# Kernel optimization log

Measured on AMD Instinct MI355X. Metric: run time of the kernel, lower is better.

## Reference

```python
import jax, jax.numpy as jnp
import numpy as np

HEADS = 8
EPS = 1e-5


def setup_inputs() -> dict:
    key = jax.random.key(0)
    ks = jax.random.split(key, 9)
    B, C, H, W = 4, 256, 128, 128
    s1 = 0.02
    inp = {
        "fmap": jax.random.normal(ks[0], (B, C, H, W), dtype=jnp.float32),
        "g": jnp.ones((C, 1, 1), dtype=jnp.float32),
        "wq1": jax.random.normal(ks[1], (C, C, 1, 1), dtype=jnp.float32) * s1,
        "wq2": jax.random.normal(ks[2], (C, 1, 3, 3), dtype=jnp.float32) * s1,
        "wk1": jax.random.normal(ks[3], (C, C, 1, 1), dtype=jnp.float32) * s1,
        "wk2": jax.random.normal(ks[4], (C, 1, 3, 3), dtype=jnp.float32) * s1,
        "wv1": jax.random.normal(ks[5], (C, C, 1, 1), dtype=jnp.float32) * s1,
        "wv2": jax.random.normal(ks[6], (C, 1, 3, 3), dtype=jnp.float32) * s1,
        "w_out": jax.random.normal(ks[7], (C, C, 1, 1), dtype=jnp.float32) * s1,
    }
    return inp


def _linear_attention(fmap, g, wq1, wq2, wk1, wk2, wv1, wv2, w_out):
    b, C, H, W = fmap.shape
    h = HEADS
    c = C // h          # head dim
    n = H * W           # tokens
    scale = c ** -0.5

    # channel LayerNorm over dim=-3 (C), learned gamma, no bias
    mean = jnp.mean(fmap, axis=1, keepdims=True)
    var = jnp.var(fmap, axis=1, keepdims=True)
    x = (fmap - mean) * jax.lax.rsqrt(var + EPS) * g[None]

    def proj(w1, w2):
        # 1x1 conv (no bias) then 3x3 depthwise conv (groups=C), SAME pad
        y = jnp.einsum('bchw,oc->bohw', x, w1[:, :, 0, 0])
        return jax.lax.conv_general_dilated(
            y, w2, window_strides=(1, 1), padding='SAME',
            dimension_numbers=('NCHW', 'OIHW', 'NCHW'),
            feature_group_count=C)

    q, k, v = proj(wq1, wq2), proj(wk1, wk2), proj(wv1, wv2)

    def to_heads(t):  # [b,C,H,W] -> [b*h, n, c]
        return t.reshape(b, h, c, n).transpose(0, 1, 3, 2).reshape(b * h, n, c)

    q, k, v = to_heads(q), to_heads(k), to_heads(v)

    q = jax.nn.softmax(q, axis=-1) * scale   # softmax over head dim
    k = jax.nn.softmax(k, axis=-2)            # softmax over tokens

    ctx = jnp.einsum('bnd,bne->bde', k, v)    # [b*h, c, c]
    out = jnp.einsum('bnd,bde->bne', q, ctx)  # [b*h, n, c]

    out = out.reshape(b, h, n, c).transpose(0, 1, 3, 2).reshape(b, C, H, W)
    out = jax.nn.silu(out)
    return jnp.einsum('bchw,oc->bohw', out, w_out[:, :, 0, 0])


def reference(fmap, g, wq1, wq2, wk1, wk2, wv1, wv2, w_out):
    return _linear_attention(fmap, g, wq1, wq2, wk1, wk2, wv1, wv2, w_out)
```

## Files before the change

kernel.cpp:

```cpp
#include <hip/hip_runtime.h>
#include <cmath>


#define B 4
#define C 256
#define Hh 128
#define Wd 128
#define HW (Hh*Wd)
#define HEADS 8
#define HD 32
#define OSCALE 256.0f
#define NSP 16

typedef _Float16 half_t;
typedef _Float16 f16x8 __attribute__((ext_vector_type(8)));
typedef float f32x4 __attribute__((ext_vector_type(4)));

__device__ __forceinline__ void gload_lds16(const half_t* g, half_t* l) {
  __builtin_amdgcn_global_load_lds((const __attribute__((address_space(1))) void*)g,
                                   (__attribute__((address_space(3))) void*)l, 16, 0, 0);
}

__global__ __launch_bounds__(256) void wcvt_all(const float* __restrict__ wq1,
                                                const float* __restrict__ wk1,
                                                const float* __restrict__ wv1,
                                                const float* __restrict__ wout,
                                                half_t* __restrict__ Wh,
                                                half_t* __restrict__ Woh,
                                                float* __restrict__ Sk) {
  int i = blockIdx.x * 256 + threadIdx.x;
  if (i < 65536) Wh[i] = (half_t)wq1[i];
  else if (i < 131072) Wh[i] = (half_t)wk1[i - 65536];
  else if (i < 196608) Wh[i] = (half_t)wv1[i - 131072];
  else Woh[i - 196608] = (half_t)wout[i - 196608];
  if (i < B * C) Sk[i] = 0.f;
}

__global__ __launch_bounds__(256) void ln2(const float* __restrict__ fmap,
                                           const float* __restrict__ g,
                                           half_t* __restrict__ Xh) {
  int b = blockIdx.y;
  int lane = threadIdx.x & 63;
  int gq = threadIdx.x >> 6;
  int px = blockIdx.x * 64 + lane;
  __shared__ float gs[C];
  __shared__ float sm1[4][64], sm2[4][64];
  gs[threadIdx.x] = g[threadIdx.x];
  const float* fp = fmap + ((size_t)b * C + gq * 64) * HW + px;
  float vbuf[64];
  float s = 0.f, s2 = 0.f;
#pragma unroll
  for (int j = 0; j < 64; ++j) {
    float v = fp[(size_t)j * HW];
    vbuf[j] = v;
    s += v; s2 = fmaf(v, v, s2);
  }
  sm1[gq][lane] = s; sm2[gq][lane] = s2;
  __syncthreads();
  float st = 0.f, st2 = 0.f;
#pragma unroll
  for (int q = 0; q < 4; ++q) { st += sm1[q][lane]; st2 += sm2[q][lane]; }
  float mean = st * (1.f / C);
  float var = st2 * (1.f / C) - mean * mean;
  float rstd = rsqrtf(var + 1e-5f);
  half_t* xp = Xh + ((size_t)b * HW + px) * 256 + gq * 64;
#pragma unroll
  for (int j0 = 0; j0 < 64; j0 += 8) {
    f16x8 v8;
#pragma unroll
    for (int jj = 0; jj < 8; ++jj)
      v8[jj] = (half_t)((vbuf[j0 + jj] - mean) * rstd * gs[gq * 64 + j0 + jj]);
    *(f16x8*)(xp + j0) = v8;
  }
}

__global__ __launch_bounds__(512) void gemm16w(const half_t* __restrict__ Xh,
                                               const half_t* __restrict__ Wh,
                                               half_t* __restrict__ Yh) {
  __shared__ __align__(16) char smem[65536];
  half_t* Xs0 = (half_t*)smem;
  half_t* Xs1 = (half_t*)(smem + 16384);
  half_t* Ws0 = (half_t*)(smem + 32768);
  half_t* Ws1 = (half_t*)(smem + 49152);
  const int tid = threadIdx.x;
  const int wave = tid >> 6, lane = tid & 63;
  const int lr = lane & 15, lq = lane >> 4;
  const int b = blockIdx.z;
  const int pix0 = blockIdx.x * 128;
  const int m0 = blockIdx.y * 128;
  const int wm = wave >> 1, wn = wave & 1;

  const half_t* xb = Xh + ((size_t)b * HW + pix0) * 256;
  const half_t* wb = Wh + (size_t)m0 * 256;

  f32x4 acc[2][4];
#pragma unroll
  for (int i = 0; i < 2; ++i)
#pragma unroll
    for (int j = 0; j < 4; ++j) { f32x4 z = {0.f, 0.f, 0.f, 0.f}; acc[i][j] = z; }

#pragma unroll
  for (int it = 0; it < 2; ++it) {
    int e = it * 512 + tid, r = e >> 3, c = e & 7;
    int go = (c ^ (r & 7)) << 3;
    gload_lds16(xb + (size_t)r * 256 + go, Xs0 + e * 8);
    gload_lds16(wb + (size_t)r * 256 + go, Ws0 + e * 8);
  }
  __syncthreads();

#pragma unroll
  for (int kk = 0; kk < 4; ++kk) {
    half_t* Xsb = (kk & 1) ? Xs1 : Xs0;
    half_t* Wsb = (kk & 1) ? Ws1 : Ws0;
    if (kk < 3) {
      half_t* Xsn = (kk & 1) ? Xs0 : Xs1;
      half_t* Wsn = (kk & 1) ? Ws0 : Ws1;
#pragma unroll
      for (int it = 0; it < 2; ++it) {
        int e = it * 512 + tid, r = e >> 3, c = e & 7;
        int go = (kk + 1) * 64 + ((c ^ (r & 7)) << 3);
        gload_lds16(xb + (size_t)r * 256 + go, Xsn + e * 8);
        gload_lds16(wb + (size_t)r * 256 + go, Wsn + e * 8);
      }
    }
#pragma unroll
    for (int kf = 0; kf < 2; ++kf) {
      f16x8 afr[2], bfr[4];
#pragma unroll
      for (int mf = 0; mf < 2; ++mf) {
        int r = wm * 32 + mf * 16 + lr;
        int q = kf * 4 + lq;
        afr[mf] = *(const f16x8*)&Wsb[r * 64 + ((q ^ (r & 7)) << 3)];
      }
#pragma unroll
      for (int nf = 0; nf < 4; ++nf) {
        int r = wn * 64 + nf * 16 + lr;
        int q = kf * 4 + lq;
        bfr[nf] = *(const f16x8*)&Xsb[r * 64 + ((q ^ (r & 7)) << 3)];
      }
#pragma unroll
      for (int mf = 0; mf < 2; ++mf)
#pragma unroll
        for (int nf = 0; nf < 4; ++nf)
          acc[mf][nf] = __builtin_amdgcn_mfma_f32_16x16x32_f16(afr[mf], bfr[nf], acc[mf][nf], 0, 0, 0);
    }
    __syncthreads();
  }

#pragma unroll
  for (int mf = 0; mf < 2; ++mf)
#pragma unroll
    for (int nf = 0; nf < 4; ++nf)
#pragma unroll
      for (int j = 0; j < 4; ++j) {
        int row = wm * 32 + mf * 16 + lq * 4 + j;
        int col = wn * 64 + nf * 16 + lr;
        int byte = row * 256 + ((col * 2) ^ ((row & 7) << 4));
        *(half_t*)(smem + byte) = (half_t)acc[mf][nf][j];
      }
  __syncthreads();
  half_t* dst_base = Yh + (size_t)(m0 >> 8) * ((size_t)B * C * HW)
                     + ((size_t)(b * C + (m0 & 255))) * HW + pix0;
#pragma unroll
  for (int it = 0; it < 4; ++it) {
    int i = it * 512 + tid;
    int row = i >> 4, ch = i & 15;
    int src = row * 256 + ((ch * 16) ^ ((row & 7) << 4));
    *(f16x8*)(dst_base + (size_t)row * HW + ch * 8) = *(const f16x8*)(smem + src);
  }
}

__global__ __launch_bounds__(256) void dw3x3_v(const half_t* __restrict__ Yin,
                                               const float* __restrict__ W2,
                                               half_t* __restrict__ Zv) {
  int c = blockIdx.y, b = blockIdx.z;
  int r = threadIdx.x >> 4;
  int j0 = (threadIdx.x & 15) * 8;
  int i = blockIdx.x * 16 + r;
  const half_t* plane = Yin + ((size_t)(b * C + c)) * HW;
  float w[9];
#pragma unroll
  for (int k = 0; k < 9; ++k) w[k] = W2[c * 9 + k];
  float acc[8];
#pragma unroll
  for (int p = 0; p < 8; ++p) acc[p] = 0.f;
#pragma unroll
  for (int dr = 0; dr < 3; ++dr) {
    int ii = i + dr - 1;
    if (ii < 0 || ii >= Hh) continue;
    const half_t* rp = plane + ii * Wd + j0;
    f16x8 cv = *(const f16x8*)rp;
    float lv = (j0 > 0) ? (float)rp[-1] : 0.f;
    float rv = (j0 + 8 < Wd) ? (float)rp[8] : 0.f;
    float cf[8];
#pragma unroll
    for (int p = 0; p < 8; ++p) cf[p] = (float)cv[p];
    float w0 = w[dr * 3], w1 = w[dr * 3 + 1], w2v = w[dr * 3 + 2];
#pragma unroll
    for (int p = 0; p < 8; ++p) {
      float l = (p == 0) ? lv : cf[p - 1];
      float rr = (p == 7) ? rv : cf[p + 1];
      acc[p] = fmaf(w0, l, acc[p]);
      acc[p] = fmaf(w1, cf[p], acc[p]);
      acc[p] = fmaf(w2v, rr, acc[p]);
    }
  }
  size_t off = ((size_t)(b * C + c)) * HW + i * Wd + j0;
  f16x8 o8;
#pragma unroll
  for (int p = 0; p < 8; ++p) o8[p] = (half_t)acc[p];
  *(f16x8*)(Zv + off) = o8;
}

__global__ __launch_bounds__(256) void dw3x3_k(const half_t* __restrict__ Yin,
                                               const float* __restrict__ W2,
                                               half_t* __restrict__ Zv,
                                               float* __restrict__ Sk) {
  int c = blockIdx.y, b = blockIdx.z;
  int r = threadIdx.x >> 4;
  int j0 = (threadIdx.x & 15) * 8;
  int i = blockIdx.x * 16 + r;
  const half_t* plane = Yin + ((size_t)(b * C + c)) * HW;
  float w[9];
#pragma unroll
  for (int k = 0; k < 9; ++k) w[k] = W2[c * 9 + k];
  float acc[8];
#pragma unroll
  for (int p = 0; p < 8; ++p) acc[p] = 0.f;
#pragma unroll
  for (int dr = 0; dr < 3; ++dr) {
    int ii = i + dr - 1;
    if (ii < 0 || ii >= Hh) continue;
    const half_t* rp = plane + ii * Wd + j0;
    f16x8 cv = *(const f16x8*)rp;
    float lv = (j0 > 0) ? (float)rp[-1] : 0.f;
    float rv = (j0 + 8 < Wd) ? (float)rp[8] : 0.f;
    float cf[8];
#pragma unroll
    for (int p = 0; p < 8; ++p) cf[p] = (float)cv[p];
    float w0 = w[dr * 3], w1 = w[dr * 3 + 1], w2v = w[dr * 3 + 2];
#pragma unroll
    for (int p = 0; p < 8; ++p) {
      float l = (p == 0) ? lv : cf[p - 1];
      float rr = (p == 7) ? rv : cf[p + 1];
      acc[p] = fmaf(w0, l, acc[p]);
      acc[p] = fmaf(w1, cf[p], acc[p]);
      acc[p] = fmaf(w2v, rr, acc[p]);
    }
  }
  size_t off = ((size_t)(b * C + c)) * HW + i * Wd + j0;
  f16x8 o8;
  float local = 0.f;
#pragma unroll
  for (int p = 0; p < 8; ++p) {
    float e = expf(acc[p]);
    o8[p] = (half_t)e;
    local += e;
  }
  *(f16x8*)(Zv + off) = o8;
  __shared__ float red[256];
  int t = threadIdx.x;
  red[t] = local; __syncthreads();
  for (int st = 128; st > 0; st >>= 1) {
    if (t < st) red[t] += red[t + st];
    __syncthreads();
  }
  if (t == 0) atomicAdd(&Sk[b * C + c], red[0]);
}

__global__ __launch_bounds__(256) void ctx_mfma(const half_t* __restrict__ EK,
                                                const half_t* __restrict__ V,
                                                float* __restrict__ part) {
  int bh = blockIdx.x, sp = blockIdx.y;
  int wave = threadIdx.x >> 6, lane = threadIdx.x & 63;
  int lr = lane & 15, lq = lane >> 4;
  const size_t base = (size_t)bh * HD * HW;
  const half_t* ekp = EK + base + (size_t)lr * HW;
  const half_t* vp  = V  + base + (size_t)lr * HW;
  f32x4 a00 = {0.f,0.f,0.f,0.f}, a01 = a00, a10 = a00, a11 = a00;
  const int n0w = sp * 1024 + wave * 256 + lq * 8;
#pragma unroll
  for (int ks = 0; ks < 8; ++ks) {
    int n = n0w + ks * 32;
    f16x8 fa0 = *(const f16x8*)(ekp + n);
    f16x8 fa1 = *(const f16x8*)(ekp + (size_t)16 * HW + n);
    f16x8 fb0 = *(const f16x8*)(vp + n);
    f16x8 fb1 = *(const f16x8*)(vp + (size_t)16 * HW + n);
    a00 = __builtin_amdgcn_mfma_f32_16x16x32_f16(fa0, fb0, a00, 0, 0, 0);
    a01 = __builtin_amdgcn_mfma_f32_16x16x32_f16(fa0, fb1, a01, 0, 0, 0);
    a10 = __builtin_amdgcn_mfma_f32_16x16x32_f16(fa1, fb0, a10, 0, 0, 0);
    a11 = __builtin_amdgcn_mfma_f32_16x16x32_f16(fa1, fb1, a11, 0, 0, 0);
  }
  __shared__ float red[4][1024];
#pragma unroll
  for (int j = 0; j < 4; ++j) {
    int dlo = lq * 4 + j;
    red[wave][(dlo)      * 32 + lr]      = a00[j];
    red[wave][(dlo)      * 32 + 16 + lr] = a01[j];
    red[wave][(dlo + 16) * 32 + lr]      = a10[j];
    red[wave][(dlo + 16) * 32 + 16 + lr] = a11[j];
  }
  __syncthreads();
  float* pp = part + ((size_t)sp * 32 + bh) * 1024;
  for (int idx = threadIdx.x; idx < 1024; idx += 256)
    pp[idx] = red[0][idx] + red[1][idx] + red[2][idx] + red[3][idx];
}

__global__ __launch_bounds__(256) void ctxred(const float* __restrict__ part,
                                              const float* __restrict__ Sk,
                                              half_t* __restrict__ ctxh) {
  int bh = blockIdx.x;
  int t = threadIdx.x;
  for (int idx = t; idx < 1024; idx += 256) {
    int d = idx >> 5, e = idx & 31;
    float s = 0.f;
#pragma unroll
    for (int sp = 0; sp < NSP; ++sp) s += part[((size_t)sp * 32 + bh) * 1024 + idx];
    ctxh[(size_t)bh * 1024 + e * 32 + d] = (half_t)(s / Sk[bh * HD + d]);
  }
}

__global__ __launch_bounds__(256) void attn6(const half_t* __restrict__ Qh,
                                             const half_t* __restrict__ ctxh,
                                             const half_t* __restrict__ Woh,
                                             float* __restrict__ outp) {
  const int b = blockIdx.y;
  const int lane = threadIdx.x & 63;
  const int w = threadIdx.x >> 6;
  const int lr = lane & 15, lq = lane >> 4;
  const int px0 = blockIdx.x * 64;
  const int px = px0 + w * 16 + lr;
  __shared__ __align__(16) char osm[64 * 512];

  {
    f16x8 cf[HEADS][2];
#pragma unroll
    for (int h = 0; h < HEADS; ++h)
#pragma unroll
      for (int eh = 0; eh < 2; ++eh)
        cf[h][eh] = *(const f16x8*)(ctxh + ((size_t)(b * HEADS + h)) * 1024
                                    + (eh * 16 + lr) * 32 + lq * 8);
    const int pxl_base = w * 16 + lq * 4;
#pragma unroll
    for (int h = 0; h < HEADS; ++h) {
      const half_t* qp = Qh + ((size_t)(b * C + h * HD + lq * 8)) * HW + px;
      float ev[8];
      float psum = 0.f;
#pragma unroll
      for (int j = 0; j < 8; ++j) {
        ev[j] = expf((float)qp[(size_t)j * HW]);
        psum += ev[j];
      }
      float s = psum;
      s += __shfl_xor(s, 16, 64);
      s += __shfl_xor(s, 32, 64);
      float inv = 0.1767766952966369f / s;
      f16x8 pa;
#pragma unroll
      for (int j = 0; j < 8; ++j) pa[j] = (half_t)(ev[j] * inv);

      f32x4 z = {0.f, 0.f, 0.f, 0.f};
      f32x4 a0 = __builtin_amdgcn_mfma_f32_16x16x32_f16(pa, cf[h][0], z, 0, 0, 0);
      f32x4 a1 = __builtin_amdgcn_mfma_f32_16x16x32_f16(pa, cf[h][1], z, 0, 0, 0);
#pragma unroll
      for (int eh = 0; eh < 2; ++eh) {
        f32x4 a = eh ? a1 : a0;
        int cc = h * 32 + eh * 16 + lr;
#pragma unroll
        for (int j = 0; j < 4; ++j) {
          int pxl = pxl_base + j;
          float v = a[j];
          float sg = 1.f / (1.f + expf(-v));
          int byte = pxl * 512 + ((cc * 2) ^ ((pxl & 7) << 4));
          *(half_t*)(osm + byte) = (half_t)(v * sg * OSCALE);
        }
      }
    }
  }
  __syncthreads();

  f32x4 acc[4][4];
#pragma unroll
  for (int i = 0; i < 4; ++i)
#pragma unroll
    for (int j = 0; j < 4; ++j) { f32x4 z = {0.f, 0.f, 0.f, 0.f}; acc[i][j] = z; }

  const half_t* wbase = Woh + ((size_t)(w * 64 + lr)) * 256 + lq * 8;
#pragma unroll
  for (int k0 = 0; k0 < 256; k0 += 32) {
    f16x8 afr[4], bfr[4];
#pragma unroll
    for (int mf = 0; mf < 4; ++mf)
      afr[mf] = *(const f16x8*)(wbase + (size_t)(mf * 16) * 256 + k0);
#pragma unroll
    for (int nf = 0; nf < 4; ++nf) {
      int r = nf * 16 + lr;
      bfr[nf] = *(const f16x8*)(osm + r * 512 + ((k0 * 2 + lq * 16) ^ ((r & 7) << 4)));
    }
#pragma unroll
    for (int mf = 0; mf < 4; ++mf)
#pragma unroll
      for (int nf = 0; nf < 4; ++nf)
        acc[mf][nf] = __builtin_amdgcn_mfma_f32_16x16x32_f16(afr[mf], bfr[nf], acc[mf][nf], 0, 0, 0);
  }

#pragma unroll
  for (int mf = 0; mf < 4; ++mf) {
    int oc = w * 64 + mf * 16 + lq * 4;
#pragma unroll
    for (int nf = 0; nf < 4; ++nf) {
      float* dst = outp + ((size_t)(b * C + oc)) * HW + px0 + nf * 16 + lr;
#pragma unroll
      for (int j = 0; j < 4; ++j)
        dst[(size_t)j * HW] = acc[mf][nf][j] * (1.0f / OSCALE);
    }
  }
}

extern "C" void kernel_launch(void* const* d_in, const int* in_sizes, int n_in,
                              void* d_out, int out_size, void* d_ws, size_t ws_size,
                              hipStream_t stream) {
  const float* fmap = (const float*)d_in[0];
  const float* g    = (const float*)d_in[1];
  const float* wq1  = (const float*)d_in[2];
  const float* wq2  = (const float*)d_in[3];
  const float* wk1  = (const float*)d_in[4];
  const float* wk2  = (const float*)d_in[5];
  const float* wv1  = (const float*)d_in[6];
  const float* wv2  = (const float*)d_in[7];
  const float* wout = (const float*)d_in[8];
  float* out = (float*)d_out;
  char* ws = (char*)d_ws;

  const size_t SZ = (size_t)B * C * HW;
  const size_t Mi = (size_t)1 << 20;
  half_t* Xh   = (half_t*)(ws);
  half_t* Yh   = (half_t*)(ws + 32 * Mi);
  half_t* Qh   = (half_t*)(ws + 128 * Mi);
  half_t* EK   = (half_t*)(ws);
  half_t* Vh   = (half_t*)out;
  float*  part = (float*)(ws + 96 * Mi);
  float*  Sk   = (float*)(ws + 160 * Mi);
  half_t* ctxh = (half_t*)(ws + 100 * Mi);
  half_t* Wh   = (half_t*)(ws + 192 * Mi);
  half_t* Woh  = (half_t*)(ws + 192 * Mi + 512 * 1024);

  wcvt_all<<<dim3(1024), 256, 0, stream>>>(wq1, wk1, wv1, wout, Wh, Woh, Sk);

  ln2<<<dim3(HW / 64, B), 256, 0, stream>>>(fmap, g, Xh);

  gemm16w<<<dim3(HW / 128, 6, B), 512, 0, stream>>>(Xh, Wh, Yh);

  dw3x3_v<<<dim3(Hh / 16, C, B), 256, 0, stream>>>(Yh, wq2, Qh);
  dw3x3_k<<<dim3(Hh / 16, C, B), 256, 0, stream>>>(Yh + SZ, wk2, EK, Sk);
  dw3x3_v<<<dim3(Hh / 16, C, B), 256, 0, stream>>>(Yh + 2 * SZ, wv2, Vh);

  ctx_mfma<<<dim3(HEADS * B, NSP), 256, 0, stream>>>(EK, Vh, part);
  ctxred<<<dim3(32), 256, 0, stream>>>(part, Sk, ctxh);

  attn6<<<dim3(HW / 64, B), 256, 0, stream>>>(Qh, ctxh, Woh, out);
}
```

Before: 209.7 us.

## Deepen QKV GEMM LDS pipeline to four stages; load attention ctx per head

Result: faster. 198.5 us (-5.4%).

```diff
diff --git a/kernel.cpp b/kernel.cpp
--- a/kernel.cpp
+++ b/kernel.cpp
@@ -74,14 +74,10 @@
   }
 }
 
-__global__ __launch_bounds__(512) void gemm16w(const half_t* __restrict__ Xh,
+__global__ __launch_bounds__(512) void gemm16r(const half_t* __restrict__ Xh,
                                                const half_t* __restrict__ Wh,
                                                half_t* __restrict__ Yh) {
   __shared__ __align__(16) char smem[65536];
-  half_t* Xs0 = (half_t*)smem;
-  half_t* Xs1 = (half_t*)(smem + 16384);
-  half_t* Ws0 = (half_t*)(smem + 32768);
-  half_t* Ws1 = (half_t*)(smem + 49152);
   const int tid = threadIdx.x;
   const int wave = tid >> 6, lane = tid & 63;
   const int lr = lane & 15, lq = lane >> 4;
@@ -99,53 +95,48 @@
 #pragma unroll
     for (int j = 0; j < 4; ++j) { f32x4 z = {0.f, 0.f, 0.f, 0.f}; acc[i][j] = z; }
 
-#pragma unroll
-  for (int it = 0; it < 2; ++it) {
-    int e = it * 512 + tid, r = e >> 3, c = e & 7;
-    int go = (c ^ (r & 7)) << 3;
-    gload_lds16(xb + (size_t)r * 256 + go, Xs0 + e * 8);
-    gload_lds16(wb + (size_t)r * 256 + go, Ws0 + e * 8);
-  }
-  __syncthreads();
-
-#pragma unroll
-  for (int kk = 0; kk < 4; ++kk) {
-    half_t* Xsb = (kk & 1) ? Xs1 : Xs0;
-    half_t* Wsb = (kk & 1) ? Ws1 : Ws0;
-    if (kk < 3) {
-      half_t* Xsn = (kk & 1) ? Xs0 : Xs1;
-      half_t* Wsn = (kk & 1) ? Ws0 : Ws1;
-#pragma unroll
-      for (int it = 0; it < 2; ++it) {
-        int e = it * 512 + tid, r = e >> 3, c = e & 7;
-        int go = (kk + 1) * 64 + ((c ^ (r & 7)) << 3);
-        gload_lds16(xb + (size_t)r * 256 + go, Xsn + e * 8);
-        gload_lds16(wb + (size_t)r * 256 + go, Wsn + e * 8);
-      }
-    }
-#pragma unroll
-    for (int kf = 0; kf < 2; ++kf) {
-      f16x8 afr[2], bfr[4];
-#pragma unroll
-      for (int mf = 0; mf < 2; ++mf) {
-        int r = wm * 32 + mf * 16 + lr;
-        int q = kf * 4 + lq;
-        afr[mf] = *(const f16x8*)&Wsb[r * 64 + ((q ^ (r & 7)) << 3)];
-      }
-#pragma unroll
-      for (int nf = 0; nf < 4; ++nf) {
-        int r = wn * 64 + nf * 16 + lr;
-        int q = kf * 4 + lq;
-        bfr[nf] = *(const f16x8*)&Xsb[r * 64 + ((q ^ (r & 7)) << 3)];
-      }
-#pragma unroll
-      for (int mf = 0; mf < 2; ++mf)
-#pragma unroll
-        for (int nf = 0; nf < 4; ++nf)
-          acc[mf][nf] = __builtin_amdgcn_mfma_f32_16x16x32_f16(afr[mf], bfr[nf], acc[mf][nf], 0, 0, 0);
-    }
-    __syncthreads();
-  }
+#define STAGE(kt, s) do {                                                       \
+    int r_ = tid >> 2, c_ = tid & 3;                                            \
+    int cs_ = c_ ^ ((r_ >> 1) & 3);                                             \
+    gload_lds16(xb + (size_t)r_ * 256 + (kt) * 32 + (cs_ << 3),                 \
+                (half_t*)(smem + (s) * 16384) + tid * 8);                       \
+    gload_lds16(wb + (size_t)r_ * 256 + (kt) * 32 + (cs_ << 3),                 \
+                (half_t*)(smem + (s) * 16384 + 8192) + tid * 8);                \
+  } while (0)
+
+  STAGE(0, 0);
+  STAGE(1, 1);
+
+#pragma unroll
+  for (int t = 0; t < 8; ++t) {
+    if (t < 6) STAGE(t + 2, (t + 2) & 3);
+    if (t < 6)       asm volatile("s_waitcnt vmcnt(4)" ::: "memory");
+    else if (t == 6) asm volatile("s_waitcnt vmcnt(2)" ::: "memory");
+    else             asm volatile("s_waitcnt vmcnt(0)" ::: "memory");
+    __builtin_amdgcn_sched_barrier(0);
+    __builtin_amdgcn_s_barrier();
+    const char* slot = smem + (t & 3) * 16384;
+    f16x8 afr[2], bfr[4];
+#pragma unroll
+    for (int mf = 0; mf < 2; ++mf) {
+      int r = wm * 32 + mf * 16 + lr;
+      afr[mf] = *(const f16x8*)(slot + 8192 + r * 64 + ((lq ^ ((r >> 1) & 3)) << 4));
+    }
+#pragma unroll
+    for (int nf = 0; nf < 4; ++nf) {
+      int r = wn * 64 + nf * 16 + lr;
+      bfr[nf] = *(const f16x8*)(slot + r * 64 + ((lq ^ ((r >> 1) & 3)) << 4));
+    }
+#pragma unroll
+    for (int mf = 0; mf < 2; ++mf)
+#pragma unroll
+      for (int nf = 0; nf < 4; ++nf)
+        acc[mf][nf] = __builtin_amdgcn_mfma_f32_16x16x32_f16(afr[mf], bfr[nf], acc[mf][nf], 0, 0, 0);
+  }
+#undef STAGE
+  asm volatile("s_waitcnt lgkmcnt(0)" ::: "memory");
+  __builtin_amdgcn_sched_barrier(0);
+  __builtin_amdgcn_s_barrier();
 
 #pragma unroll
   for (int mf = 0; mf < 2; ++mf)
@@ -320,10 +311,10 @@
   }
 }
 
-__global__ __launch_bounds__(256) void attn6(const half_t* __restrict__ Qh,
-                                             const half_t* __restrict__ ctxh,
-                                             const half_t* __restrict__ Woh,
-                                             float* __restrict__ outp) {
+__global__ __launch_bounds__(256) void attn6b(const half_t* __restrict__ Qh,
+                                              const half_t* __restrict__ ctxh,
+                                              const half_t* __restrict__ Woh,
+                                              float* __restrict__ outp) {
   const int b = blockIdx.y;
   const int lane = threadIdx.x & 63;
   const int w = threadIdx.x >> 6;
@@ -333,16 +324,13 @@
   __shared__ __align__(16) char osm[64 * 512];
 
   {
-    f16x8 cf[HEADS][2];
-#pragma unroll
-    for (int h = 0; h < HEADS; ++h)
-#pragma unroll
-      for (int eh = 0; eh < 2; ++eh)
-        cf[h][eh] = *(const f16x8*)(ctxh + ((size_t)(b * HEADS + h)) * 1024
-                                    + (eh * 16 + lr) * 32 + lq * 8);
     const int pxl_base = w * 16 + lq * 4;
 #pragma unroll
     for (int h = 0; h < HEADS; ++h) {
+      const half_t* cb = ctxh + ((size_t)(b * HEADS + h)) * 1024;
+      f16x8 cf0 = *(const f16x8*)(cb + (lr)      * 32 + lq * 8);
+      f16x8 cf1 = *(const f16x8*)(cb + (16 + lr) * 32 + lq * 8);
+
       const half_t* qp = Qh + ((size_t)(b * C + h * HD + lq * 8)) * HW + px;
       float ev[8];
       float psum = 0.f;
@@ -360,8 +348,8 @@
       for (int j = 0; j < 8; ++j) pa[j] = (half_t)(ev[j] * inv);
 
       f32x4 z = {0.f, 0.f, 0.f, 0.f};
-      f32x4 a0 = __builtin_amdgcn_mfma_f32_16x16x32_f16(pa, cf[h][0], z, 0, 0, 0);
-      f32x4 a1 = __builtin_amdgcn_mfma_f32_16x16x32_f16(pa, cf[h][1], z, 0, 0, 0);
+      f32x4 a0 = __builtin_amdgcn_mfma_f32_16x16x32_f16(pa, cf0, z, 0, 0, 0);
+      f32x4 a1 = __builtin_amdgcn_mfma_f32_16x16x32_f16(pa, cf1, z, 0, 0, 0);
 #pragma unroll
       for (int eh = 0; eh < 2; ++eh) {
         f32x4 a = eh ? a1 : a0;
@@ -449,7 +437,7 @@
 
   ln2<<<dim3(HW / 64, B), 256, 0, stream>>>(fmap, g, Xh);
 
-  gemm16w<<<dim3(HW / 128, 6, B), 512, 0, stream>>>(Xh, Wh, Yh);
+  gemm16r<<<dim3(HW / 128, 6, B), 512, 0, stream>>>(Xh, Wh, Yh);
 
   dw3x3_v<<<dim3(Hh / 16, C, B), 256, 0, stream>>>(Yh, wq2, Qh);
   dw3x3_k<<<dim3(Hh / 16, C, B), 256, 0, stream>>>(Yh + SZ, wk2, EK, Sk);
@@ -458,5 +446,5 @@
   ctx_mfma<<<dim3(HEADS * B, NSP), 256, 0, stream>>>(EK, Vh, part);
   ctxred<<<dim3(32), 256, 0, stream>>>(part, Sk, ctxh);
 
-  attn6<<<dim3(HW / 64, B), 256, 0, stream>>>(Qh, ctxh, Woh, out);
-}
+  attn6b<<<dim3(HW / 64, B), 256, 0, stream>>>(Qh, ctxh, Woh, out);
+}
```
